# Kernel tuning notes

Measured on AMD Instinct MI355X. Metric: run time of the kernel, lower is better.

Reference implementation:

```python
import jax, jax.numpy as jnp
import numpy as np

N_ATOMS = 500000
MUL0, MUL1, MUL2 = 32, 16, 8      # geometry/output multiplicities for 0e,1o,2e
FMUL0, FMUL1 = 32, 16             # field multiplicities for 0e,1o

# real Wigner 3j for (1,1,2) in e3nn real basis order (l=1: y,z,x ; l=2: xy,yz,z2,zx,x2-y2)
# orthonormal symmetric-traceless basis matrices / sqrt(5) so that sum of squares == 1
def _w3j_112():
    s2 = 1.0 / np.sqrt(2.0); s6 = 1.0 / np.sqrt(6.0)
    C = np.zeros((3, 3, 5), np.float32)
    C[0, 2, 0] = C[2, 0, 0] = s2            # xy
    C[0, 1, 1] = C[1, 0, 1] = s2            # yz
    C[1, 1, 2] = 2.0 * s6; C[0, 0, 2] = -s6; C[2, 2, 2] = -s6  # z2
    C[1, 2, 3] = C[2, 1, 3] = s2            # zx
    C[2, 2, 4] = s2; C[0, 0, 4] = -s2       # x2-y2
    return C / np.sqrt(5.0)

W3J112 = jnp.asarray(_w3j_112())
INV_S3 = float(1.0 / np.sqrt(3.0))   # w3j(0,l,l) = I/sqrt(2l+1), w3j(1,1,0) = I/sqrt(3)
INV_S5 = float(1.0 / np.sqrt(5.0))   # w3j(2,0,2) = I/sqrt(5)
# e3nn FullyConnectedTensorProduct path coefficients (component irrep_normalization, element path_normalization):
# sqrt((2*l_out+1) / sum over paths with same output of mul1*mul2)
C0 = float(np.sqrt(1.0 / (MUL0 * FMUL0 + MUL1 * FMUL1)))          # -> 0e : 1/sqrt(1280)
C1 = float(np.sqrt(3.0 / (MUL0 * FMUL1 + MUL1 * FMUL0 + MUL2 * FMUL1)))  # -> 1o : sqrt(3/1152)
C2 = float(np.sqrt(5.0 / (MUL1 * FMUL1 + MUL2 * FMUL0)))          # -> 2e : sqrt(5/512)


def _forward(geometry_features, field_features,
             w_000, w_011, w_101, w_110, w_112, w_202, w_211,
             wl0, wl1, wl2):
    n = geometry_features.shape[0]
    g0 = geometry_features[:, :32]                       # (n, 32)
    g1 = geometry_features[:, 32:80].reshape(n, 16, 3)   # (n, 16, 3)
    g2 = geometry_features[:, 80:120].reshape(n, 8, 5)   # (n, 8, 5)
    f0 = field_features[:32]                             # (32,)  global, broadcast over atoms
    f1 = field_features[32:].reshape(16, 3)              # (16, 3)

    # --- tensor product paths (uvw connection mode) ---
    out0 = C0 * (jnp.einsum('uvw,zu,v->zw', w_000, g0, f0)
                 + INV_S3 * jnp.einsum('uvw,zui,vi->zw', w_110, g1, f1))
    out1 = C1 * (INV_S3 * jnp.einsum('uvw,zu,vk->zwk', w_011, g0, f1)
                 + INV_S3 * jnp.einsum('uvw,zuk,v->zwk', w_101, g1, f0)
                 + jnp.einsum('uvw,ijk,zuk,vi->zwj', w_211, W3J112, g2, f1))
    out2 = C2 * (jnp.einsum('uvw,ijk,zui,vj->zwk', w_112, W3J112, g1, f1)
                 + INV_S5 * jnp.einsum('uvw,zuk,v->zwk', w_202, g2, f0))

    # --- residual o3.Linear (matching irreps only, 1/sqrt(fan_in)) ---
    r0 = jnp.einsum('uw,zu->zw', wl0, g0) * float(1.0 / np.sqrt(MUL0))
    r1 = jnp.einsum('uw,zui->zwi', wl1, g1) * float(1.0 / np.sqrt(MUL1))
    r2 = jnp.einsum('uw,zui->zwi', wl2, g2) * float(1.0 / np.sqrt(MUL2))

    return jnp.concatenate([out0 + r0,
                            (out1 + r1).reshape(n, 48),
                            (out2 + r2).reshape(n, 40)], axis=1)


def setup_inputs() -> dict:
    key = jax.random.key(0)
    ks = jax.random.split(key, 12)
    rn = lambda k, s: jax.random.normal(k, s, dtype=jnp.float32)
    return {
        'geometry_features': rn(ks[0], (N_ATOMS, 120)),
        'field_features': rn(ks[1], (80,)),
        'w_000': rn(ks[2], (32, 32, 32)),  # (0e,0e)->0e
        'w_011': rn(ks[3], (32, 16, 16)),  # (0e,1o)->1o
        'w_101': rn(ks[4], (16, 32, 16)),  # (1o,0e)->1o
        'w_110': rn(ks[5], (16, 16, 32)),  # (1o,1o)->0e
        'w_112': rn(ks[6], (16, 16, 8)),   # (1o,1o)->2e
        'w_202': rn(ks[7], (8, 32, 8)),    # (2e,0e)->2e
        'w_211': rn(ks[8], (8, 16, 16)),   # (2e,1o)->1o
        'wl0': rn(ks[9], (32, 32)),
        'wl1': rn(ks[10], (16, 16)),
        'wl2': rn(ks[11], (8, 8)),
    }


def reference(geometry_features, field_features,
              w_000, w_011, w_101, w_110, w_112, w_202, w_211,
              wl0, wl1, wl2):
    return _forward(geometry_features, field_features,
                    w_000, w_011, w_101, w_110, w_112, w_202, w_211,
                    wl0, wl1, wl2)
```

## Files before the change

### kernel.cpp

```cpp
#include <hip/hip_runtime.h>

#define LDA 136
#define TM  64
#define CST 132

__constant__ float W3J[45] = {
  0.f, 0.f, -0.18257418583505536f, 0.f, -0.31622776601683794f,
  0.f, 0.31622776601683794f, 0.f, 0.f, 0.f,
  0.31622776601683794f, 0.f, 0.f, 0.f, 0.f,
  0.f, 0.31622776601683794f, 0.f, 0.f, 0.f,
  0.f, 0.f, 0.36514837167011072f, 0.f, 0.f,
  0.f, 0.f, 0.f, 0.31622776601683794f, 0.f,
  0.31622776601683794f, 0.f, 0.f, 0.f, 0.f,
  0.f, 0.f, 0.f, 0.31622776601683794f, 0.f,
  0.f, 0.f, -0.18257418583505536f, 0.f, 0.31622776601683794f
};

__device__ __forceinline__ unsigned short f2bf(float f) {
  unsigned int u = __float_as_uint(f);
  u += 0x7FFFu + ((u >> 16) & 1u);
  return (unsigned short)(u >> 16);
}

__global__ void build_B_kernel(
    const float* __restrict__ field,
    const float* __restrict__ w000, const float* __restrict__ w011,
    const float* __restrict__ w101, const float* __restrict__ w110,
    const float* __restrict__ w112, const float* __restrict__ w202,
    const float* __restrict__ w211, const float* __restrict__ wl0,
    const float* __restrict__ wl1,  const float* __restrict__ wl2,
    unsigned short* __restrict__ Bt)
{
  const float C0  = 0.02795084971874737f;
  const float C1  = 0.051031036307982884f;
  const float C2  = 0.09882117688026186f;
  const float IS3 = 0.57735026918962576f;
  const float IS5 = 0.44721359549995794f;

  int n = blockIdx.x;
  int k = threadIdx.x;
  float val = 0.0f;

  if (n < 120 && k < 120) {
    if (n < 32) {
      int w = n;
      if (k < 32) {
        int u = k;
        float a = 0.f;
        for (int v = 0; v < 32; ++v) a += w000[u*1024 + v*32 + w] * field[v];
        val = C0 * a + wl0[u*32 + w] * 0.17677669529663689f;
      } else if (k < 80) {
        int u = (k-32)/3, i = (k-32)%3;
        float a = 0.f;
        for (int v = 0; v < 16; ++v) a += w110[u*512 + v*32 + w] * field[32 + v*3 + i];
        val = C0 * IS3 * a;
      }
    } else if (n < 80) {
      int w = (n-32)/3, j = (n-32)%3;
      if (k < 32) {
        int u = k;
        float a = 0.f;
        for (int v = 0; v < 16; ++v) a += w011[u*256 + v*16 + w] * field[32 + v*3 + j];
        val = C1 * IS3 * a;
      } else if (k < 80) {
        int u = (k-32)/3, i = (k-32)%3;
        if (i == j) {
          float a = 0.f;
          for (int v = 0; v < 32; ++v) a += w101[u*512 + v*16 + w] * field[v];
          val = C1 * IS3 * a + wl1[u*16 + w] * 0.25f;
        }
      } else {
        int u = (k-80)/5, kk = (k-80)%5;
        float c0w = W3J[0*15 + j*5 + kk];
        float c1w = W3J[1*15 + j*5 + kk];
        float c2w = W3J[2*15 + j*5 + kk];
        float a = 0.f;
        for (int v = 0; v < 16; ++v) {
          float s = c0w*field[32+v*3+0] + c1w*field[32+v*3+1] + c2w*field[32+v*3+2];
          a += w211[u*256 + v*16 + w] * s;
        }
        val = C1 * a;
      }
    } else {
      int w = (n-80)/5, k2 = (n-80)%5;
      if (k >= 32 && k < 80) {
        int u = (k-32)/3, i = (k-32)%3;
        float c0w = W3J[i*15 + 0*5 + k2];
        float c1w = W3J[i*15 + 1*5 + k2];
        float c2w = W3J[i*15 + 2*5 + k2];
        float a = 0.f;
        for (int v = 0; v < 16; ++v) {
          float s = c0w*field[32+v*3+0] + c1w*field[32+v*3+1] + c2w*field[32+v*3+2];
          a += w112[u*128 + v*8 + w] * s;
        }
        val = C2 * a;
      } else if (k >= 80) {
        int u = (k-80)/5, kk = (k-80)%5;
        if (kk == k2) {
          float a = 0.f;
          for (int v = 0; v < 32; ++v) a += w202[u*256 + v*8 + w] * field[v];
          val = C2 * IS5 * a + wl2[u*8 + w] * 0.35355339059327378f;
        }
      }
    }
  }
  Bt[n*128 + k] = f2bf(val);
}

typedef __attribute__((ext_vector_type(8))) __bf16 bf16x8;
typedef __attribute__((ext_vector_type(4))) float  f32x4;

__global__ __launch_bounds__(256, 4) void coupling_main(
    const float* __restrict__ geom, const unsigned short* __restrict__ Btg,
    float* __restrict__ out, int natoms)
{
  __shared__ alignas(16) unsigned char smem[128 * LDA * 2];
  unsigned short* Bl = (unsigned short*)smem;
  float*          Cl = (float*)smem;

  int tid = threadIdx.x;
  long long base = (long long)blockIdx.x * TM;

  int lane = tid & 63;
  int wave = tid >> 6;
  int mrow = lane & 15;
  int kq   = lane >> 4;

  long long atomA = base + wave * 16 + mrow;
  bool ina = (atomA < natoms);
  const float* ga = geom + atomA * 120 + kq * 8;
  float4 alo[4], ahi[4];
  #pragma unroll
  for (int ks = 0; ks < 4; ++ks) {
    bool pad = (ks == 3) && (kq == 3);
    if (ina && !pad) {
      alo[ks] = ((const float4*)(ga + ks * 32))[0];
      ahi[ks] = ((const float4*)(ga + ks * 32))[1];
    } else {
      alo[ks] = make_float4(0.f, 0.f, 0.f, 0.f);
      ahi[ks] = make_float4(0.f, 0.f, 0.f, 0.f);
    }
  }

  #pragma unroll
  for (int r = 0; r < 8; ++r) {
    int g   = tid + r * 256;
    int row = g >> 4;
    int col = (g & 15) * 8;
    uint4 v = ((const uint4*)Btg)[g];
    *((uint4*)&Bl[row * LDA + col]) = v;
  }

  bf16x8 af[4];
  #pragma unroll
  for (int ks = 0; ks < 4; ++ks) {
    uint4 pk;
    pk.x = ((unsigned)f2bf(alo[ks].y) << 16) | f2bf(alo[ks].x);
    pk.y = ((unsigned)f2bf(alo[ks].w) << 16) | f2bf(alo[ks].z);
    pk.z = ((unsigned)f2bf(ahi[ks].y) << 16) | f2bf(ahi[ks].x);
    pk.w = ((unsigned)f2bf(ahi[ks].w) << 16) | f2bf(ahi[ks].z);
    af[ks] = __builtin_bit_cast(bf16x8, pk);
  }

  __syncthreads();

  f32x4 zero = {0.f, 0.f, 0.f, 0.f};
  f32x4 acc[8];
  #pragma unroll
  for (int t = 0; t < 8; ++t) acc[t] = zero;

  const unsigned short* brow = &Bl[mrow * LDA + kq * 8];

  #pragma unroll
  for (int ks = 0; ks < 4; ++ks) {
    #pragma unroll
    for (int t = 0; t < 8; ++t) {
      bf16x8 bf_ = __builtin_bit_cast(bf16x8, *(const uint4*)(brow + t * 16 * LDA + ks * 32));
      acc[t] = __builtin_amdgcn_mfma_f32_16x16x32_bf16(af[ks], bf_, acc[t], 0, 0, 0);
    }
  }

  __syncthreads();

  int crow = wave * 16 + kq * 4;
  #pragma unroll
  for (int t = 0; t < 8; ++t) {
    int n = t * 16 + mrow;
    #pragma unroll
    for (int r2 = 0; r2 < 4; ++r2) {
      Cl[(crow + r2) * CST + n] = acc[t][r2];
    }
  }
  __syncthreads();

  #pragma unroll
  for (int r = 0; r < 8; ++r) {
    int g = tid + r * 256;
    if (g < 1920) {
      int row = g / 30;
      int c4  = g - row * 30;
      long long atom = base + row;
      if (atom < natoms) {
        f32x4 v = *(const f32x4*)&Cl[row * CST + c4 * 4];
        __builtin_nontemporal_store(v, (f32x4*)(out + atom * 120 + c4 * 4));
      }
    }
  }
}

extern "C" void kernel_launch(void* const* d_in, const int* in_sizes, int n_in,
                              void* d_out, int out_size, void* d_ws, size_t ws_size,
                              hipStream_t stream) {
  const float* geom  = (const float*)d_in[0];
  const float* field = (const float*)d_in[1];
  const float* w000  = (const float*)d_in[2];
  const float* w011  = (const float*)d_in[3];
  const float* w101  = (const float*)d_in[4];
  const float* w110  = (const float*)d_in[5];
  const float* w112  = (const float*)d_in[6];
  const float* w202  = (const float*)d_in[7];
  const float* w211  = (const float*)d_in[8];
  const float* wl0   = (const float*)d_in[9];
  const float* wl1   = (const float*)d_in[10];
  const float* wl2   = (const float*)d_in[11];
  float* out = (float*)d_out;
  unsigned short* Bt = (unsigned short*)d_ws;

  int natoms = in_sizes[0] / 120;

  build_B_kernel<<<dim3(128), dim3(128), 0, stream>>>(
      field, w000, w011, w101, w110, w112, w202, w211, wl0, wl1, wl2, Bt);

  int ntiles = (natoms + TM - 1) / TM;
  coupling_main<<<dim3(ntiles), dim3(256), 0, stream>>>(geom, Bt, out, natoms);
}
```

Baseline: 423.2 us.

## Use persistent grid-stride blocks with register prefetch and direct output stores

The main kernel becomes persistent: 1024 blocks loop over atom tiles and load the B matrix into shared memory only once per block. Each iteration prefetches the next tile's geometry rows into registers while the current tile's MFMAs run. The shared-memory staging of C is dropped, and results are written with scalar nontemporal stores straight from the accumulators. This removes repeated B loads and two barriers per tile, but the scattered 4-byte stores may coalesce worse than the earlier 16-byte row stores.

```diff
diff --git a/kernel.cpp b/kernel.cpp
--- a/kernel.cpp
+++ b/kernel.cpp
@@ -2,7 +2,6 @@
 
 #define LDA 136
 #define TM  64
-#define CST 132
 
 __constant__ float W3J[45] = {
   0.f, 0.f, -0.18257418583505536f, 0.f, -0.31622776601683794f,
@@ -112,35 +111,15 @@
 
 __global__ __launch_bounds__(256, 4) void coupling_main(
     const float* __restrict__ geom, const unsigned short* __restrict__ Btg,
-    float* __restrict__ out, int natoms)
+    float* __restrict__ out, int natoms, int ntiles)
 {
-  __shared__ alignas(16) unsigned char smem[128 * LDA * 2];
-  unsigned short* Bl = (unsigned short*)smem;
-  float*          Cl = (float*)smem;
-
-  int tid = threadIdx.x;
-  long long base = (long long)blockIdx.x * TM;
-
-  int lane = tid & 63;
-  int wave = tid >> 6;
-  int mrow = lane & 15;
-  int kq   = lane >> 4;
-
-  long long atomA = base + wave * 16 + mrow;
-  bool ina = (atomA < natoms);
-  const float* ga = geom + atomA * 120 + kq * 8;
-  float4 alo[4], ahi[4];
-  #pragma unroll
-  for (int ks = 0; ks < 4; ++ks) {
-    bool pad = (ks == 3) && (kq == 3);
-    if (ina && !pad) {
-      alo[ks] = ((const float4*)(ga + ks * 32))[0];
-      ahi[ks] = ((const float4*)(ga + ks * 32))[1];
-    } else {
-      alo[ks] = make_float4(0.f, 0.f, 0.f, 0.f);
-      ahi[ks] = make_float4(0.f, 0.f, 0.f, 0.f);
-    }
-  }
+  __shared__ alignas(16) unsigned short Bl[128 * LDA];
+
+  const int tid  = threadIdx.x;
+  const int lane = tid & 63;
+  const int wave = tid >> 6;
+  const int mrow = lane & 15;
+  const int kq   = lane >> 4;
 
   #pragma unroll
   for (int r = 0; r < 8; ++r) {
@@ -151,60 +130,106 @@
     *((uint4*)&Bl[row * LDA + col]) = v;
   }
 
-  bf16x8 af[4];
-  #pragma unroll
-  for (int ks = 0; ks < 4; ++ks) {
-    uint4 pk;
-    pk.x = ((unsigned)f2bf(alo[ks].y) << 16) | f2bf(alo[ks].x);
-    pk.y = ((unsigned)f2bf(alo[ks].w) << 16) | f2bf(alo[ks].z);
-    pk.z = ((unsigned)f2bf(ahi[ks].y) << 16) | f2bf(ahi[ks].x);
-    pk.w = ((unsigned)f2bf(ahi[ks].w) << 16) | f2bf(ahi[ks].z);
-    af[ks] = __builtin_bit_cast(bf16x8, pk);
+  const int rowin = wave * 16 + mrow;
+  int tile = blockIdx.x;
+  const int stride = gridDim.x;
+  const float4 f0 = make_float4(0.f, 0.f, 0.f, 0.f);
+
+  float4 alo[4], ahi[4];
+
+  if (tile < ntiles) {
+    long long atom = (long long)tile * TM + rowin;
+    const float* ga = geom + atom * 120 + kq * 8;
+    bool full = ((long long)tile * TM + TM) <= natoms;
+    bool ina  = full || (atom < natoms);
+    #pragma unroll
+    for (int ks = 0; ks < 4; ++ks) {
+      bool pad = (ks == 3) && (kq == 3);
+      if (ina && !pad) {
+        alo[ks] = ((const float4*)(ga + ks * 32))[0];
+        ahi[ks] = ((const float4*)(ga + ks * 32))[1];
+      } else {
+        alo[ks] = f0; ahi[ks] = f0;
+      }
+    }
+  } else {
+    #pragma unroll
+    for (int ks = 0; ks < 4; ++ks) { alo[ks] = f0; ahi[ks] = f0; }
   }
 
   __syncthreads();
 
-  f32x4 zero = {0.f, 0.f, 0.f, 0.f};
-  f32x4 acc[8];
-  #pragma unroll
-  for (int t = 0; t < 8; ++t) acc[t] = zero;
-
   const unsigned short* brow = &Bl[mrow * LDA + kq * 8];
 
-  #pragma unroll
-  for (int ks = 0; ks < 4; ++ks) {
-    #pragma unroll
-    for (int t = 0; t < 8; ++t) {
-      bf16x8 bf_ = __builtin_bit_cast(bf16x8, *(const uint4*)(brow + t * 16 * LDA + ks * 32));
-      acc[t] = __builtin_amdgcn_mfma_f32_16x16x32_bf16(af[ks], bf_, acc[t], 0, 0, 0);
-    }
-  }
-
-  __syncthreads();
-
-  int crow = wave * 16 + kq * 4;
-  #pragma unroll
-  for (int t = 0; t < 8; ++t) {
-    int n = t * 16 + mrow;
-    #pragma unroll
-    for (int r2 = 0; r2 < 4; ++r2) {
-      Cl[(crow + r2) * CST + n] = acc[t][r2];
-    }
-  }
-  __syncthreads();
-
-  #pragma unroll
-  for (int r = 0; r < 8; ++r) {
-    int g = tid + r * 256;
-    if (g < 1920) {
-      int row = g / 30;
-      int c4  = g - row * 30;
-      long long atom = base + row;
-      if (atom < natoms) {
-        f32x4 v = *(const f32x4*)&Cl[row * CST + c4 * 4];
-        __builtin_nontemporal_store(v, (f32x4*)(out + atom * 120 + c4 * 4));
-      }
-    }
+  while (tile < ntiles) {
+    const int next = tile + stride;
+    const long long tbase = (long long)tile * TM;
+
+    bf16x8 af[4];
+    #pragma unroll
+    for (int ks = 0; ks < 4; ++ks) {
+      uint4 pk;
+      pk.x = ((unsigned)f2bf(alo[ks].y) << 16) | f2bf(alo[ks].x);
+      pk.y = ((unsigned)f2bf(alo[ks].w) << 16) | f2bf(alo[ks].z);
+      pk.z = ((unsigned)f2bf(ahi[ks].y) << 16) | f2bf(ahi[ks].x);
+      pk.w = ((unsigned)f2bf(ahi[ks].w) << 16) | f2bf(ahi[ks].z);
+      af[ks] = __builtin_bit_cast(bf16x8, pk);
+    }
+
+    if (next < ntiles) {
+      long long atom = (long long)next * TM + rowin;
+      const float* ga = geom + atom * 120 + kq * 8;
+      bool full = ((long long)next * TM + TM) <= natoms;
+      bool ina  = full || (atom < natoms);
+      #pragma unroll
+      for (int ks = 0; ks < 4; ++ks) {
+        bool pad = (ks == 3) && (kq == 3);
+        if (ina && !pad) {
+          alo[ks] = ((const float4*)(ga + ks * 32))[0];
+          ahi[ks] = ((const float4*)(ga + ks * 32))[1];
+        } else {
+          alo[ks] = f0; ahi[ks] = f0;
+        }
+      }
+    }
+
+    f32x4 acc[8];
+    #pragma unroll
+    for (int t = 0; t < 8; ++t) acc[t] = (f32x4){0.f, 0.f, 0.f, 0.f};
+    #pragma unroll
+    for (int ks = 0; ks < 4; ++ks) {
+      #pragma unroll
+      for (int t = 0; t < 8; ++t) {
+        bf16x8 bf_ = __builtin_bit_cast(bf16x8, *(const uint4*)(brow + t * 16 * LDA + ks * 32));
+        acc[t] = __builtin_amdgcn_mfma_f32_16x16x32_bf16(af[ks], bf_, acc[t], 0, 0, 0);
+      }
+    }
+
+    long long atom0 = tbase + wave * 16 + kq * 4;
+    if (tbase + TM <= natoms) {
+      #pragma unroll
+      for (int t = 0; t < 8; ++t) {
+        int n = t * 16 + mrow;
+        if (n < 120) {
+          #pragma unroll
+          for (int r2 = 0; r2 < 4; ++r2)
+            __builtin_nontemporal_store(acc[t][r2], out + (atom0 + r2) * 120 + n);
+        }
+      }
+    } else {
+      #pragma unroll
+      for (int t = 0; t < 8; ++t) {
+        int n = t * 16 + mrow;
+        if (n < 120) {
+          #pragma unroll
+          for (int r2 = 0; r2 < 4; ++r2)
+            if (atom0 + r2 < natoms)
+              __builtin_nontemporal_store(acc[t][r2], out + (atom0 + r2) * 120 + n);
+        }
+      }
+    }
+
+    tile = next;
   }
 }
 
@@ -232,5 +257,6 @@
       field, w000, w011, w101, w110, w112, w202, w211, wl0, wl1, wl2, Bt);
 
   int ntiles = (natoms + TM - 1) / TM;
-  coupling_main<<<dim3(ntiles), dim3(256), 0, stream>>>(geom, Bt, out, natoms);
-}
+  int nblk = ntiles < 1024 ? ntiles : 1024;
+  coupling_main<<<dim3(nblk), dim3(256), 0, stream>>>(geom, Bt, out, natoms, ntiles);
+}
```

Result: slower. 524.5 us (+23.9%).
